# Optimization experiments

Hardware: AMD Instinct MI355X
Metric: run time of the kernel (lower is better)

Reference implementation:

```python
import jax, jax.numpy as jnp
import numpy as np

ORDER = 5
LOOKAHEAD = 2
N_DF_BINS = 96
N_FREQ_BINS = 481
B, T = 32, 1000


def setup_inputs() -> dict:
    key = jax.random.key(0)
    k1, k2, k3 = jax.random.split(key, 3)
    spec = jax.random.normal(k1, (B, 1, T, N_FREQ_BINS, 2), dtype=jnp.float32)
    coefs = jax.random.normal(k2, (B, T, ORDER, N_DF_BINS, 2), dtype=jnp.float32)
    alpha = jax.random.uniform(k3, (B, T, 1), dtype=jnp.float32)
    return {"spec": spec, "coefs": coefs, "alpha": alpha}


def reference(spec, coefs, alpha):
    b, _, t, _, _ = spec.shape
    f = N_DF_BINS
    # [b, t, f, 2] slice of the deep-filtered bins
    x = spec[:, 0, :, :f, :]
    # causal-ish pad along time: (order - lookahead - 1) left, lookahead right
    xp = jnp.pad(x, ((0, 0), (ORDER - LOOKAHEAD - 1, LOOKAHEAD), (0, 0), (0, 0)))
    # stack the `order` shifted time windows -> [b, order, t, f, 2]
    w = jnp.stack([jax.lax.dynamic_slice_in_dim(xp, i, t, axis=1) for i in range(ORDER)], axis=1)
    # coefs [b, t, order, f, 2] -> [b, order, t, f, 2]
    c = jnp.swapaxes(coefs, 1, 2)
    # complex multiply-accumulate over the filter order
    re = jnp.sum(w[..., 0] * c[..., 0] - w[..., 1] * c[..., 1], axis=1)  # [b, t, f]
    im = jnp.sum(w[..., 1] * c[..., 0] + w[..., 0] * c[..., 1], axis=1)  # [b, t, f]
    spec_f = jnp.stack([re, im], axis=-1)[:, None]  # [b, 1, t, f, 2]
    # assign_df with alpha blending on the first f bins
    a = alpha.reshape(b, 1, -1, 1, 1)
    blend = spec_f * a + spec[..., :f, :] * (1.0 - a)
    return spec.at[..., :f, :].set(blend)
```

## Files before the change

kernel.cpp:

```cpp
#include <hip/hip_runtime.h>


typedef float f2 __attribute__((ext_vector_type(2)));
typedef float f4 __attribute__((ext_vector_type(4)));

#define ORDER 5
#define TPAD  2
#define NDF   96
#define NF    481
#define TT    1000
#define BB    32
#define NROWS (BB * TT)
#define ROWF  (NF * 2)
#define CROWF (ORDER * NDF * 2)

__global__ __launch_bounds__(256) void df_kernel(
    const float* __restrict__ spec,
    const float* __restrict__ coefs,
    const float* __restrict__ alpha,
    float* __restrict__ out)
{
    const int bid = blockIdx.x;
    const int row = (bid & 7) * (NROWS / 8) + (bid >> 3);
    const int t   = row % TT;
    const int tid = threadIdx.x;

    const float* __restrict__ srow = spec + (size_t)row * ROWF;
    float* __restrict__       orow = out  + (size_t)row * ROWF;

    if (tid < 48) {
        const float* __restrict__ crow = coefs + (size_t)row * CROWF;
        const float a   = alpha[row];
        const float oma = 1.0f - a;

        float re0 = 0.f, im0 = 0.f, re1 = 0.f, im1 = 0.f;
        f2 s0, s1;
#pragma unroll
        for (int i = 0; i < ORDER; ++i) {
            const int ts = t + i - TPAD;
            if (ts >= 0 && ts < TT) {
                const float* w = spec + (size_t)(row + i - TPAD) * ROWF + 4 * tid;
                const f2 w0 = *(const f2*)(w);
                const f2 w1 = *(const f2*)(w + 2);
                const f4 c = __builtin_nontemporal_load(
                    (const f4*)(crow + i * (NDF * 2) + 4 * tid));
                re0 += w0.x * c.x - w0.y * c.y;
                im0 += w0.y * c.x + w0.x * c.y;
                re1 += w1.x * c.z - w1.y * c.w;
                im1 += w1.y * c.z + w1.x * c.w;
                if (i == TPAD) { s0 = w0; s1 = w1; }
            }
        }
        f2 o0, o1;
        o0.x = re0 * a + s0.x * oma;  o0.y = im0 * a + s0.y * oma;
        o1.x = re1 * a + s1.x * oma;  o1.y = im1 * a + s1.y * oma;
        __builtin_nontemporal_store(o0, (f2*)(orow + 4 * tid));
        __builtin_nontemporal_store(o1, (f2*)(orow + 4 * tid + 2));
    } else {
        if ((row & 1) == 0) {
            if (tid < 240) {
                const int k = tid - 48;
                const f4 v = __builtin_nontemporal_load((const f4*)(srow + 192 + 4 * k));
                __builtin_nontemporal_store(v, (f4*)(orow + 192 + 4 * k));
            } else if (tid == 240) {
                const f2 v = __builtin_nontemporal_load((const f2*)(srow + 960));
                __builtin_nontemporal_store(v, (f2*)(orow + 960));
            }
        } else {
            if (tid == 48) {
                const f2 v = __builtin_nontemporal_load((const f2*)(srow + 192));
                __builtin_nontemporal_store(v, (f2*)(orow + 192));
            } else if (tid < 241) {
                const int k = tid - 49;
                const f4 v = __builtin_nontemporal_load((const f4*)(srow + 194 + 4 * k));
                __builtin_nontemporal_store(v, (f4*)(orow + 194 + 4 * k));
            }
        }
    }
}

extern "C" void kernel_launch(void* const* d_in, const int* in_sizes, int n_in,
                              void* d_out, int out_size, void* d_ws, size_t ws_size,
                              hipStream_t stream) {
    const float* spec  = (const float*)d_in[0];
    const float* coefs = (const float*)d_in[1];
    const float* alpha = (const float*)d_in[2];
    float* out = (float*)d_out;

    dim3 grid(NROWS);
    dim3 block(256);
    df_kernel<<<grid, block, 0, stream>>>(spec, coefs, alpha, out);
}
```

Measured before the change: 288.6 us.

## Split kernel into separate copy blocks and multi-row deep-filter blocks

New measurement: 297.2 us. 1.03x slower.

```diff
diff --git a/kernel.cpp b/kernel.cpp
--- a/kernel.cpp
+++ b/kernel.cpp
@@ -14,66 +14,74 @@
 #define ROWF  (NF * 2)
 #define CROWF (ORDER * NDF * 2)
 
+#define TAILF2   385
+#define COPY_U   (NROWS * TAILF2)
+#define CPB      6400
+#define NCOPY    (COPY_U / CPB)
+
+#define RPB      25
+#define NDFB     (NROWS / RPB)
+
 __global__ __launch_bounds__(256) void df_kernel(
     const float* __restrict__ spec,
     const float* __restrict__ coefs,
     const float* __restrict__ alpha,
     float* __restrict__ out)
 {
-    const int bid = blockIdx.x;
-    const int row = (bid & 7) * (NROWS / 8) + (bid >> 3);
-    const int t   = row % TT;
     const int tid = threadIdx.x;
 
-    const float* __restrict__ srow = spec + (size_t)row * ROWF;
-    float* __restrict__       orow = out  + (size_t)row * ROWF;
+    if (blockIdx.x < NCOPY) {
+        const unsigned base = (unsigned)blockIdx.x * CPB + tid;
+#pragma unroll 5
+        for (int it = 0; it < CPB / 256; ++it) {
+            const unsigned u   = base + it * 256;
+            const unsigned row = u / TAILF2;
+            const unsigned k   = u - row * TAILF2;
+            const float* sp = spec + (size_t)row * ROWF + 192 + 2 * k;
+            float*       op = out  + (size_t)row * ROWF + 192 + 2 * k;
+            const f2 v = __builtin_nontemporal_load((const f2*)sp);
+            __builtin_nontemporal_store(v, (f2*)op);
+        }
+    } else {
+        const int db   = blockIdx.x - NCOPY;
+        const int lane = tid % 48;
+        const int ro   = tid / 48;
+        if (ro < 5) {
+            const int r0 = db * RPB;
+#pragma unroll
+            for (int it = 0; it < RPB / 5; ++it) {
+                const int row = r0 + it * 5 + ro;
+                const int t   = row % TT;
+                const float* __restrict__ srow = spec  + (size_t)row * ROWF;
+                const float* __restrict__ crow = coefs + (size_t)row * CROWF;
+                float*       __restrict__ orow = out   + (size_t)row * ROWF;
 
-    if (tid < 48) {
-        const float* __restrict__ crow = coefs + (size_t)row * CROWF;
-        const float a   = alpha[row];
-        const float oma = 1.0f - a;
+                const float a   = alpha[row];
+                const float oma = 1.0f - a;
 
-        float re0 = 0.f, im0 = 0.f, re1 = 0.f, im1 = 0.f;
-        f2 s0, s1;
+                float re0 = 0.f, im0 = 0.f, re1 = 0.f, im1 = 0.f;
+                f2 s0 = {0.f, 0.f}, s1 = {0.f, 0.f};
 #pragma unroll
-        for (int i = 0; i < ORDER; ++i) {
-            const int ts = t + i - TPAD;
-            if (ts >= 0 && ts < TT) {
-                const float* w = spec + (size_t)(row + i - TPAD) * ROWF + 4 * tid;
-                const f2 w0 = *(const f2*)(w);
-                const f2 w1 = *(const f2*)(w + 2);
-                const f4 c = __builtin_nontemporal_load(
-                    (const f4*)(crow + i * (NDF * 2) + 4 * tid));
-                re0 += w0.x * c.x - w0.y * c.y;
-                im0 += w0.y * c.x + w0.x * c.y;
-                re1 += w1.x * c.z - w1.y * c.w;
-                im1 += w1.y * c.z + w1.x * c.w;
-                if (i == TPAD) { s0 = w0; s1 = w1; }
-            }
-        }
-        f2 o0, o1;
-        o0.x = re0 * a + s0.x * oma;  o0.y = im0 * a + s0.y * oma;
-        o1.x = re1 * a + s1.x * oma;  o1.y = im1 * a + s1.y * oma;
-        __builtin_nontemporal_store(o0, (f2*)(orow + 4 * tid));
-        __builtin_nontemporal_store(o1, (f2*)(orow + 4 * tid + 2));
-    } else {
-        if ((row & 1) == 0) {
-            if (tid < 240) {
-                const int k = tid - 48;
-                const f4 v = __builtin_nontemporal_load((const f4*)(srow + 192 + 4 * k));
-                __builtin_nontemporal_store(v, (f4*)(orow + 192 + 4 * k));
-            } else if (tid == 240) {
-                const f2 v = __builtin_nontemporal_load((const f2*)(srow + 960));
-                __builtin_nontemporal_store(v, (f2*)(orow + 960));
-            }
-        } else {
-            if (tid == 48) {
-                const f2 v = __builtin_nontemporal_load((const f2*)(srow + 192));
-                __builtin_nontemporal_store(v, (f2*)(orow + 192));
-            } else if (tid < 241) {
-                const int k = tid - 49;
-                const f4 v = __builtin_nontemporal_load((const f4*)(srow + 194 + 4 * k));
-                __builtin_nontemporal_store(v, (f4*)(orow + 194 + 4 * k));
+                for (int i = 0; i < ORDER; ++i) {
+                    const int ts = t + i - TPAD;
+                    if (ts >= 0 && ts < TT) {
+                        const float* w = spec + (size_t)(row + i - TPAD) * ROWF + 4 * lane;
+                        const f2 w0 = *(const f2*)(w);
+                        const f2 w1 = *(const f2*)(w + 2);
+                        const f4 c  = __builtin_nontemporal_load(
+                            (const f4*)(crow + i * (NDF * 2) + 4 * lane));
+                        re0 += w0.x * c.x - w0.y * c.y;
+                        im0 += w0.y * c.x + w0.x * c.y;
+                        re1 += w1.x * c.z - w1.y * c.w;
+                        im1 += w1.y * c.z + w1.x * c.w;
+                        if (i == TPAD) { s0 = w0; s1 = w1; }
+                    }
+                }
+                f2 o0, o1;
+                o0.x = re0 * a + s0.x * oma;  o0.y = im0 * a + s0.y * oma;
+                o1.x = re1 * a + s1.x * oma;  o1.y = im1 * a + s1.y * oma;
+                __builtin_nontemporal_store(o0, (f2*)(orow + 4 * lane));
+                __builtin_nontemporal_store(o1, (f2*)(orow + 4 * lane + 2));
             }
         }
     }
@@ -87,7 +95,7 @@
     const float* alpha = (const float*)d_in[2];
     float* out = (float*)d_out;
 
-    dim3 grid(NROWS);
+    dim3 grid(NCOPY + NDFB);
     dim3 block(256);
     df_kernel<<<grid, block, 0, stream>>>(spec, coefs, alpha, out);
 }
```
